# Performance work log

Measured on AMD Instinct MI355X. Metric: run time of the kernel, lower is better.

The kernel has to match this reference:

```python
import jax, jax.numpy as jnp
import numpy as np

N_NODES = 50000


def _sage_conv(x, src, dst, Wl, bl, Wr):
    # mean aggregation of source-node features into target nodes
    agg = jax.ops.segment_sum(x[src], dst, num_segments=N_NODES)      # [N, C]
    deg = jax.ops.segment_sum(jnp.ones_like(src, dtype=x.dtype), dst,
                              num_segments=N_NODES)                   # [N]
    mean = agg / jnp.maximum(deg, 1.0)[:, None]
    # PyG SAGEConv: lin_l(aggr) (with bias) + lin_r(x) (no bias)
    return mean @ Wl.T + bl + x @ Wr.T


def setup_inputs() -> dict:
    key = jax.random.key(0)
    ks = jax.random.split(key, 8)
    C = 128
    E = 600000
    scale = 1.0 / np.sqrt(C)
    x = jax.random.normal(ks[0], (N_NODES, C), dtype=jnp.float32)
    edge_index = jax.random.randint(ks[1], (2, E), 0, N_NODES, dtype=jnp.int64)
    Wl1 = jax.random.normal(ks[2], (C, C), dtype=jnp.float32) * scale
    bl1 = jnp.zeros((C,), dtype=jnp.float32)
    Wr1 = jax.random.normal(ks[3], (C, C), dtype=jnp.float32) * scale
    Wl2 = jax.random.normal(ks[4], (C, C), dtype=jnp.float32) * scale
    bl2 = jnp.zeros((C,), dtype=jnp.float32)
    Wr2 = jax.random.normal(ks[5], (C, C), dtype=jnp.float32) * scale
    return {"x": x, "edge_index": edge_index, "Wl1": Wl1, "bl1": bl1,
            "Wr1": Wr1, "Wl2": Wl2, "bl2": bl2, "Wr2": Wr2}


def reference(x, edge_index, Wl1, bl1, Wr1, Wl2, bl2, Wr2):
    src, dst = edge_index[0], edge_index[1]
    h = _sage_conv(x, src, dst, Wl1, bl1, Wr1)
    h = jax.nn.relu(h)
    out = _sage_conv(h, src, dst, Wl2, bl2, Wr2)
    return out
```

## Files before the change

kernel.cpp:

```cpp
#include <hip/hip_runtime.h>
#include <hip/hip_bf16.h>

#define N_NODES 50000
#define C 128
#define NPAD 50176
#define NTILES (NPAD / 16)
#define GEMM_BLOCKS (NTILES / 8)
#define SCAN1_BLOCKS (NPAD / 256)
#define XPREP_BLOCKS 3125
#define WPREP_BLOCKS 256

typedef short bf16x8 __attribute__((ext_vector_type(8)));
typedef float f32x4 __attribute__((ext_vector_type(4)));

__device__ __forceinline__ unsigned short f2bf(float f) {
    unsigned int u = __float_as_uint(f);
    unsigned int r = u + 0x7fffu + ((u >> 16) & 1u);
    return (unsigned short)(r >> 16);
}

__device__ __forceinline__ float bf2f(unsigned short b) {
    return __uint_as_float(((unsigned int)b) << 16);
}

__global__ __launch_bounds__(256) void build_kernel(
    const int* __restrict__ dst, int* __restrict__ deg, int E, int edgeBlocks,
    const float* __restrict__ x, unsigned short* __restrict__ Xb,
    const float* __restrict__ Wl1, const float* __restrict__ Wr1,
    const float* __restrict__ Wl2, const float* __restrict__ Wr2,
    unsigned short* __restrict__ Wc1, unsigned short* __restrict__ Wc2) {
    int b = blockIdx.x;
    if (b < edgeBlocks) {
        int e = b * 256 + threadIdx.x;
        if (e < E) {
            int d = dst[e];
            if ((unsigned)d < (unsigned)N_NODES) atomicAdd(deg + d, 1);
        }
    } else if (b < edgeBlocks + XPREP_BLOCKS) {
        int t = (b - edgeBlocks) * 256 + threadIdx.x;
        if (t >= N_NODES * C / 8) return;
        const float4 a = *(const float4*)(x + (size_t)t * 8);
        const float4 c = *(const float4*)(x + (size_t)t * 8 + 4);
        unsigned short o[8] = {f2bf(a.x), f2bf(a.y), f2bf(a.z), f2bf(a.w),
                               f2bf(c.x), f2bf(c.y), f2bf(c.z), f2bf(c.w)};
        *(uint4*)(Xb + (size_t)t * 8) = *(const uint4*)o;
    } else {
        int idx = (b - edgeBlocks - XPREP_BLOCKS) * 256 + threadIdx.x;
        int layer = idx >> 15;
        int r = idx & 32767;
        int j = r >> 8, k = r & 255;
        const float* Wl = layer ? Wl2 : Wl1;
        const float* Wr = layer ? Wr2 : Wr1;
        unsigned short* Wc = layer ? Wc2 : Wc1;
        float f = (k < 128) ? Wl[j * 128 + k] : Wr[j * 128 + (k - 128)];
        Wc[r] = f2bf(f);
    }
}

__global__ __launch_bounds__(256) void scan1_kernel(const int* __restrict__ deg,
                                                    int* __restrict__ scanbuf,
                                                    int* __restrict__ blocksum) {
    int i = blockIdx.x * 256 + threadIdx.x;
    int v = (i < N_NODES) ? deg[i] : 0;
    int lane = threadIdx.x & 63;
    int wv = threadIdx.x >> 6;
    int s = v;
#pragma unroll
    for (int off = 1; off < 64; off <<= 1) {
        int t = __shfl_up(s, off, 64);
        if (lane >= off) s += t;
    }
    __shared__ int wsum[4];
    if (lane == 63) wsum[wv] = s;
    __syncthreads();
    int woff = 0;
#pragma unroll
    for (int k = 0; k < 4; ++k) woff += (k < wv) ? wsum[k] : 0;
    scanbuf[i] = s + woff - v;
    if (threadIdx.x == 255) blocksum[blockIdx.x] = s + woff;
}

__global__ __launch_bounds__(256) void scan2_kernel(const int* __restrict__ blocksum,
                                                    int* __restrict__ blockoff) {
    int t = threadIdx.x;
    int v = (t < SCAN1_BLOCKS) ? blocksum[t] : 0;
    int lane = t & 63, wv = t >> 6;
    int s = v;
#pragma unroll
    for (int off = 1; off < 64; off <<= 1) {
        int tmp = __shfl_up(s, off, 64);
        if (lane >= off) s += tmp;
    }
    __shared__ int wsum[4];
    if (lane == 63) wsum[wv] = s;
    __syncthreads();
    int woff = 0;
#pragma unroll
    for (int k = 0; k < 4; ++k) woff += (k < wv) ? wsum[k] : 0;
    if (t < SCAN1_BLOCKS) blockoff[t] = s + woff - v;
}


__global__ void fill_kernel(const int* __restrict__ src, const int* __restrict__ dst,
                            const int* __restrict__ scanbuf, const int* __restrict__ blockoff,
                            int* __restrict__ cursor, int* __restrict__ csr_src, int E) {
    int e = blockIdx.x * 256 + threadIdx.x;
    if (e < E) {
        int d = dst[e];
        int s = src[e];
        if ((unsigned)d < (unsigned)N_NODES && (unsigned)s < (unsigned)N_NODES) {
            int rp = scanbuf[d] + blockoff[d >> 8];
            int pos = rp + atomicAdd(cursor + d, 1);
            csr_src[pos] = s;
        }
    }
}

__global__ __launch_bounds__(256) void gather_kernel(
    const unsigned short* __restrict__ feat,
    const int* __restrict__ scanbuf, const int* __restrict__ blockoff,
    const int* __restrict__ csr_src, unsigned short* __restrict__ Fm) {
    int w = (blockIdx.x * 256 + threadIdx.x) >> 6;
    int lane = threadIdx.x & 63;
    if (w >= N_NODES) return;
    const int beg = scanbuf[w] + blockoff[w >> 8];
    const int end = scanbuf[w + 1] + blockoff[(w + 1) >> 8];
    const int deg = end - beg;
    float ax = 0.f, ay = 0.f;
    const unsigned short* fp = feat + lane * 2;
    for (int base = beg; base < end; base += 64) {
        const int cnt = min(64, end - base);
        int myidx = 0;
        if (lane < cnt) myidx = csr_src[base + lane];
        int j = 0;
        for (; j + 3 < cnt; j += 4) {
            int s0 = __shfl(myidx, j);
            int s1 = __shfl(myidx, j + 1);
            int s2 = __shfl(myidx, j + 2);
            int s3 = __shfl(myidx, j + 3);
            unsigned int u0 = *(const unsigned int*)(fp + (size_t)s0 * C);
            unsigned int u1 = *(const unsigned int*)(fp + (size_t)s1 * C);
            unsigned int u2 = *(const unsigned int*)(fp + (size_t)s2 * C);
            unsigned int u3 = *(const unsigned int*)(fp + (size_t)s3 * C);
            ax += bf2f((unsigned short)u0) + bf2f((unsigned short)u1) +
                  bf2f((unsigned short)u2) + bf2f((unsigned short)u3);
            ay += bf2f((unsigned short)(u0 >> 16)) + bf2f((unsigned short)(u1 >> 16)) +
                  bf2f((unsigned short)(u2 >> 16)) + bf2f((unsigned short)(u3 >> 16));
        }
        for (; j < cnt; ++j) {
            int s0 = __shfl(myidx, j);
            unsigned int u0 = *(const unsigned int*)(fp + (size_t)s0 * C);
            ax += bf2f((unsigned short)u0);
            ay += bf2f((unsigned short)(u0 >> 16));
        }
    }
    const float inv = 1.0f / fmaxf((float)deg, 1.0f);
    unsigned int mpack = (unsigned)f2bf(ax * inv) | ((unsigned)f2bf(ay * inv) << 16);
    *(unsigned int*)(Fm + (size_t)w * C + lane * 2) = mpack;
}

__global__ __launch_bounds__(256) void sage_gemm(
    const unsigned short* __restrict__ Fm,
    const unsigned short* __restrict__ Self,
    const unsigned short* __restrict__ Wc,
    const float* __restrict__ bias,
    void* __restrict__ outv, int relu, int obf16) {
    __shared__ unsigned short wl[128 * 264];
    for (int cidx = threadIdx.x; cidx < 4096; cidx += 256) {
        int row = cidx >> 5, chunk = cidx & 31;
        const uint4 v = *(const uint4*)(Wc + row * 256 + chunk * 8);
        *(uint4*)(&wl[row * 264 + chunk * 8]) = v;
    }
    __syncthreads();

    const int wave = threadIdx.x >> 6;
    const int lane = threadIdx.x & 63;
    const int m = lane & 15;
    const int q = lane >> 4;
    const int tile0 = blockIdx.x * 8 + wave * 2;

    const size_t rowoff = (size_t)(tile0 * 16 + m) * C + q * 8;
    const unsigned short* am = Fm + rowoff;
    const unsigned short* as = Self + rowoff;

    f32x4 acc[2][8];
#pragma unroll
    for (int t = 0; t < 2; ++t)
#pragma unroll
        for (int j = 0; j < 8; ++j) acc[t][j] = (f32x4){0.f, 0.f, 0.f, 0.f};

#pragma unroll
    for (int kt = 0; kt < 8; ++kt) {
        const unsigned short* A = (kt < 4) ? am : as;
        const int ko = (kt & 3) * 32;
        bf16x8 af0 = *(const bf16x8*)(A + ko);
        bf16x8 af1 = *(const bf16x8*)(A + 16 * C + ko);
#pragma unroll
        for (int jt = 0; jt < 8; ++jt) {
            bf16x8 bfrag = *(const bf16x8*)(&wl[(jt * 16 + m) * 264 + kt * 32 + q * 8]);
            acc[0][jt] = __builtin_amdgcn_mfma_f32_16x16x32_bf16(af0, bfrag, acc[0][jt], 0, 0, 0);
            acc[1][jt] = __builtin_amdgcn_mfma_f32_16x16x32_bf16(af1, bfrag, acc[1][jt], 0, 0, 0);
        }
    }

#pragma unroll
    for (int t = 0; t < 2; ++t) {
        int rbase = (tile0 + t) * 16 + q * 4;
#pragma unroll
        for (int r = 0; r < 4; ++r) {
            int row = rbase + r;
            if (row < N_NODES) {
#pragma unroll
                for (int jt = 0; jt < 8; ++jt) {
                    int col = jt * 16 + m;
                    float v = acc[t][jt][r] + bias[col];
                    if (relu) v = fmaxf(v, 0.0f);
                    if (obf16)
                        ((unsigned short*)outv)[(size_t)row * C + col] = f2bf(v);
                    else
                        ((float*)outv)[(size_t)row * C + col] = v;
                }
            }
        }
    }
}

extern "C" void kernel_launch(void* const* d_in, const int* in_sizes, int n_in,
                              void* d_out, int out_size, void* d_ws, size_t ws_size,
                              hipStream_t stream) {
    const float* x = (const float*)d_in[0];
    const int* edge = (const int*)d_in[1];
    const float* Wl1 = (const float*)d_in[2];
    const float* bl1 = (const float*)d_in[3];
    const float* Wr1 = (const float*)d_in[4];
    const float* Wl2 = (const float*)d_in[5];
    const float* bl2 = (const float*)d_in[6];
    const float* Wr2 = (const float*)d_in[7];
    float* out = (float*)d_out;

    const int E = in_sizes[1] / 2;
    const int* src = edge;
    const int* dst = edge + E;

    char* ws = (char*)d_ws;
    size_t off = 0;
    int* deg = (int*)(ws + off);              off += (size_t)N_NODES * 4;
    int* cursor = (int*)(ws + off);           off += (size_t)N_NODES * 4;
    off = (off + 511) & ~511ull;
    int* scanbuf = (int*)(ws + off);          off += ((size_t)NPAD * 4 + 511) & ~511ull;
    int* blocksum = (int*)(ws + off);         off += 512 * 4;
    int* blockoff = (int*)(ws + off);         off += 512 * 4;
    int* csr_src = (int*)(ws + off);          off += ((size_t)E * 4 + 511) & ~511ull;
    unsigned short* Xb = (unsigned short*)(ws + off); off += (size_t)NPAD * C * 2;
    unsigned short* Fm = (unsigned short*)(ws + off); off += (size_t)NPAD * C * 2;
    unsigned short* h  = (unsigned short*)(ws + off); off += (size_t)NPAD * C * 2;
    unsigned short* Wc1 = (unsigned short*)(ws + off); off += 128 * 256 * 2;
    unsigned short* Wc2 = (unsigned short*)(ws + off); off += 128 * 256 * 2;
    (void)ws_size;

    const int edgeBlocks = (E + 255) / 256;
    const int gatherBlocks = (NPAD * 64) / 256;

    hipMemsetAsync(deg, 0, (size_t)N_NODES * 8, stream);
    build_kernel<<<edgeBlocks + XPREP_BLOCKS + WPREP_BLOCKS, 256, 0, stream>>>(
        dst, deg, E, edgeBlocks, x, Xb, Wl1, Wr1, Wl2, Wr2, Wc1, Wc2);
    scan1_kernel<<<SCAN1_BLOCKS, 256, 0, stream>>>(deg, scanbuf, blocksum);
    scan2_kernel<<<1, 256, 0, stream>>>(blocksum, blockoff);
    fill_kernel<<<edgeBlocks, 256, 0, stream>>>(src, dst, scanbuf, blockoff, cursor, csr_src, E);

    gather_kernel<<<gatherBlocks, 256, 0, stream>>>(Xb, scanbuf, blockoff, csr_src, Fm);
    sage_gemm<<<GEMM_BLOCKS, 256, 0, stream>>>(Fm, Xb, Wc1, bl1, h, 1, 1);

    gather_kernel<<<gatherBlocks, 256, 0, stream>>>(h, scanbuf, blockoff, csr_src, Fm);
    sage_gemm<<<GEMM_BLOCKS, 256, 0, stream>>>(Fm, h, Wc2, bl2, out, 0, 0);
}
```

Measured before the change: 244.3 us.

## Fuse neighbor-mean gather into SAGE GEMM via shared-memory mean tile

Merges the gather and GEMM kernels into one per-layer kernel. Each wave aggregates the mean features for its 32 rows into LDS, two nodes at a time over a combined edge range with 8-way unrolled loads, then runs the MFMA GEMM reading the mean from LDS and the weights straight from global memory instead of staging them in LDS. This removes the Fm round trip through global memory and two launches per forward. The cost is far fewer waves doing the gather (GEMM_BLOCKS×4 waves instead of one wave per node), so less latency hiding for the random gathers and more serial work per wave, plus weight fragments fetched from global/L2 on every iteration.

```diff
diff --git a/kernel.cpp b/kernel.cpp
--- a/kernel.cpp
+++ b/kernel.cpp
@@ -116,72 +116,73 @@
     }
 }
 
-__global__ __launch_bounds__(256) void gather_kernel(
+__global__ __launch_bounds__(256) void fused_layer(
     const unsigned short* __restrict__ feat,
     const int* __restrict__ scanbuf, const int* __restrict__ blockoff,
-    const int* __restrict__ csr_src, unsigned short* __restrict__ Fm) {
-    int w = (blockIdx.x * 256 + threadIdx.x) >> 6;
-    int lane = threadIdx.x & 63;
-    if (w >= N_NODES) return;
-    const int beg = scanbuf[w] + blockoff[w >> 8];
-    const int end = scanbuf[w + 1] + blockoff[(w + 1) >> 8];
-    const int deg = end - beg;
-    float ax = 0.f, ay = 0.f;
-    const unsigned short* fp = feat + lane * 2;
-    for (int base = beg; base < end; base += 64) {
-        const int cnt = min(64, end - base);
-        int myidx = 0;
-        if (lane < cnt) myidx = csr_src[base + lane];
-        int j = 0;
-        for (; j + 3 < cnt; j += 4) {
-            int s0 = __shfl(myidx, j);
-            int s1 = __shfl(myidx, j + 1);
-            int s2 = __shfl(myidx, j + 2);
-            int s3 = __shfl(myidx, j + 3);
-            unsigned int u0 = *(const unsigned int*)(fp + (size_t)s0 * C);
-            unsigned int u1 = *(const unsigned int*)(fp + (size_t)s1 * C);
-            unsigned int u2 = *(const unsigned int*)(fp + (size_t)s2 * C);
-            unsigned int u3 = *(const unsigned int*)(fp + (size_t)s3 * C);
-            ax += bf2f((unsigned short)u0) + bf2f((unsigned short)u1) +
-                  bf2f((unsigned short)u2) + bf2f((unsigned short)u3);
-            ay += bf2f((unsigned short)(u0 >> 16)) + bf2f((unsigned short)(u1 >> 16)) +
-                  bf2f((unsigned short)(u2 >> 16)) + bf2f((unsigned short)(u3 >> 16));
-        }
-        for (; j < cnt; ++j) {
-            int s0 = __shfl(myidx, j);
-            unsigned int u0 = *(const unsigned int*)(fp + (size_t)s0 * C);
-            ax += bf2f((unsigned short)u0);
-            ay += bf2f((unsigned short)(u0 >> 16));
-        }
-    }
-    const float inv = 1.0f / fmaxf((float)deg, 1.0f);
-    unsigned int mpack = (unsigned)f2bf(ax * inv) | ((unsigned)f2bf(ay * inv) << 16);
-    *(unsigned int*)(Fm + (size_t)w * C + lane * 2) = mpack;
-}
-
-__global__ __launch_bounds__(256) void sage_gemm(
-    const unsigned short* __restrict__ Fm,
-    const unsigned short* __restrict__ Self,
+    const int* __restrict__ csr_src,
     const unsigned short* __restrict__ Wc,
     const float* __restrict__ bias,
     void* __restrict__ outv, int relu, int obf16) {
-    __shared__ unsigned short wl[128 * 264];
-    for (int cidx = threadIdx.x; cidx < 4096; cidx += 256) {
-        int row = cidx >> 5, chunk = cidx & 31;
-        const uint4 v = *(const uint4*)(Wc + row * 256 + chunk * 8);
-        *(uint4*)(&wl[row * 264 + chunk * 8]) = v;
-    }
-    __syncthreads();
-
+    __shared__ unsigned short smean[128 * 136];
     const int wave = threadIdx.x >> 6;
     const int lane = threadIdx.x & 63;
+    const int tile0 = blockIdx.x * 8 + wave * 2;
+    const int row0 = tile0 * 16;
+    const int lrow0 = wave * 32;
+
+    const unsigned short* fp = feat + lane * 2;
+    for (int r = 0; r < 32; r += 2) {
+        const int n0 = row0 + r;
+        if (n0 >= N_NODES) {
+            *(unsigned int*)(&smean[(lrow0 + r) * 136 + lane * 2]) = 0u;
+            *(unsigned int*)(&smean[(lrow0 + r + 1) * 136 + lane * 2]) = 0u;
+            continue;
+        }
+        const int beg0 = scanbuf[n0] + blockoff[n0 >> 8];
+        const int mid  = scanbuf[n0 + 1] + blockoff[(n0 + 1) >> 8];
+        const int end1 = scanbuf[n0 + 2] + blockoff[(n0 + 2) >> 8];
+        float ax0 = 0.f, ay0 = 0.f, ax1 = 0.f, ay1 = 0.f;
+        for (int base = beg0; base < end1; base += 64) {
+            const int cnt = min(64, end1 - base);
+            int myidx = (lane < cnt) ? csr_src[base + lane] : 0;
+            int j = 0;
+            for (; j + 7 < cnt; j += 8) {
+                unsigned int u[8];
+#pragma unroll
+                for (int l = 0; l < 8; ++l) {
+                    int s = __shfl(myidx, j + l);
+                    u[l] = *(const unsigned int*)(fp + (size_t)s * C);
+                }
+#pragma unroll
+                for (int l = 0; l < 8; ++l) {
+                    float vx = bf2f((unsigned short)u[l]);
+                    float vy = bf2f((unsigned short)(u[l] >> 16));
+                    if (base + j + l < mid) { ax0 += vx; ay0 += vy; }
+                    else                    { ax1 += vx; ay1 += vy; }
+                }
+            }
+            for (; j < cnt; ++j) {
+                int s = __shfl(myidx, j);
+                unsigned int uu = *(const unsigned int*)(fp + (size_t)s * C);
+                float vx = bf2f((unsigned short)uu);
+                float vy = bf2f((unsigned short)(uu >> 16));
+                if (base + j < mid) { ax0 += vx; ay0 += vy; }
+                else                { ax1 += vx; ay1 += vy; }
+            }
+        }
+        const float inv0 = 1.0f / fmaxf((float)(mid - beg0), 1.0f);
+        const float inv1 = 1.0f / fmaxf((float)(end1 - mid), 1.0f);
+        unsigned int p0 = (unsigned)f2bf(ax0 * inv0) | ((unsigned)f2bf(ay0 * inv0) << 16);
+        unsigned int p1 = (unsigned)f2bf(ax1 * inv1) | ((unsigned)f2bf(ay1 * inv1) << 16);
+        *(unsigned int*)(&smean[(lrow0 + r) * 136 + lane * 2]) = p0;
+        *(unsigned int*)(&smean[(lrow0 + r + 1) * 136 + lane * 2]) = p1;
+    }
+    __syncthreads();
+
     const int m = lane & 15;
     const int q = lane >> 4;
-    const int tile0 = blockIdx.x * 8 + wave * 2;
-
-    const size_t rowoff = (size_t)(tile0 * 16 + m) * C + q * 8;
-    const unsigned short* am = Fm + rowoff;
-    const unsigned short* as = Self + rowoff;
+    const unsigned short* as = feat + (size_t)(row0 + m) * C + q * 8;
+    const unsigned short* lm = &smean[(lrow0 + m) * 136 + q * 8];
 
     f32x4 acc[2][8];
 #pragma unroll
@@ -191,13 +192,18 @@
 
 #pragma unroll
     for (int kt = 0; kt < 8; ++kt) {
-        const unsigned short* A = (kt < 4) ? am : as;
-        const int ko = (kt & 3) * 32;
-        bf16x8 af0 = *(const bf16x8*)(A + ko);
-        bf16x8 af1 = *(const bf16x8*)(A + 16 * C + ko);
+        bf16x8 af0, af1;
+        if (kt < 4) {
+            af0 = *(const bf16x8*)(lm + kt * 32);
+            af1 = *(const bf16x8*)(lm + 16 * 136 + kt * 32);
+        } else {
+            const int ko = (kt - 4) * 32;
+            af0 = *(const bf16x8*)(as + ko);
+            af1 = *(const bf16x8*)(as + 16 * C + ko);
+        }
 #pragma unroll
         for (int jt = 0; jt < 8; ++jt) {
-            bf16x8 bfrag = *(const bf16x8*)(&wl[(jt * 16 + m) * 264 + kt * 32 + q * 8]);
+            bf16x8 bfrag = *(const bf16x8*)(Wc + (jt * 16 + m) * 256 + kt * 32 + q * 8);
             acc[0][jt] = __builtin_amdgcn_mfma_f32_16x16x32_bf16(af0, bfrag, acc[0][jt], 0, 0, 0);
             acc[1][jt] = __builtin_amdgcn_mfma_f32_16x16x32_bf16(af1, bfrag, acc[1][jt], 0, 0, 0);
         }
@@ -252,14 +258,12 @@
     int* blockoff = (int*)(ws + off);         off += 512 * 4;
     int* csr_src = (int*)(ws + off);          off += ((size_t)E * 4 + 511) & ~511ull;
     unsigned short* Xb = (unsigned short*)(ws + off); off += (size_t)NPAD * C * 2;
-    unsigned short* Fm = (unsigned short*)(ws + off); off += (size_t)NPAD * C * 2;
     unsigned short* h  = (unsigned short*)(ws + off); off += (size_t)NPAD * C * 2;
     unsigned short* Wc1 = (unsigned short*)(ws + off); off += 128 * 256 * 2;
     unsigned short* Wc2 = (unsigned short*)(ws + off); off += 128 * 256 * 2;
     (void)ws_size;
 
     const int edgeBlocks = (E + 255) / 256;
-    const int gatherBlocks = (NPAD * 64) / 256;
 
     hipMemsetAsync(deg, 0, (size_t)N_NODES * 8, stream);
     build_kernel<<<edgeBlocks + XPREP_BLOCKS + WPREP_BLOCKS, 256, 0, stream>>>(
@@ -268,9 +272,8 @@
     scan2_kernel<<<1, 256, 0, stream>>>(blocksum, blockoff);
     fill_kernel<<<edgeBlocks, 256, 0, stream>>>(src, dst, scanbuf, blockoff, cursor, csr_src, E);
 
-    gather_kernel<<<gatherBlocks, 256, 0, stream>>>(Xb, scanbuf, blockoff, csr_src, Fm);
-    sage_gemm<<<GEMM_BLOCKS, 256, 0, stream>>>(Fm, Xb, Wc1, bl1, h, 1, 1);
-
-    gather_kernel<<<gatherBlocks, 256, 0, stream>>>(h, scanbuf, blockoff, csr_src, Fm);
-    sage_gemm<<<GEMM_BLOCKS, 256, 0, stream>>>(Fm, h, Wc2, bl2, out, 0, 0);
-}
+    fused_layer<<<GEMM_BLOCKS, 256, 0, stream>>>(Xb, scanbuf, blockoff, csr_src,
+                                                 Wc1, bl1, h, 1, 1);
+    fused_layer<<<GEMM_BLOCKS, 256, 0, stream>>>(h, scanbuf, blockoff, csr_src,
+                                                 Wc2, bl2, out, 0, 0);
+}
```

Result: slower. 322.8 us (+32.2%).

## Fuse whole GNN pipeline into one cooperative persistent kernel with grid syncs

Applied to the files above, without the earlier changes.

Replaces the eight separate launches plus memset with a single cooperative kernel of 512 blocks that steps through each stage in grid-stride loops separated by grid.sync(). The aim is to remove per-launch overhead and the idle gaps between the many small stages. It also unrolls the gather loop to 8 loads in flight and reads GEMM weight fragments straight from global memory instead of staging them in LDS. Risks are the cost of grid-wide barriers, lower parallelism in the gather phases from the fixed grid, and non-LDS weight reads. If the cooperative launch fails, the old multi-kernel path still runs.

```diff
diff --git a/kernel.cpp b/kernel.cpp
--- a/kernel.cpp
+++ b/kernel.cpp
@@ -1,12 +1,20 @@
 #include <hip/hip_runtime.h>
 #include <hip/hip_bf16.h>
+#include <hip/hip_cooperative_groups.h>
+
+namespace cg = cooperative_groups;
 
 #define N_NODES 50000
 #define C 128
 #define NPAD 50176
 #define NTILES (NPAD / 16)
 #define GEMM_BLOCKS (NTILES / 8)
-#define SCAN1_BLOCKS (NPAD / 256)
+#define SCAN_CHUNKS (NPAD / 256)
+#define GRID 512
+#define GWAVES (GRID * 4)
+#define XCHUNKS (N_NODES * C / 8)
+#define WITEMS (2 * 128 * 256)
+#define SCAN1_BLOCKS SCAN_CHUNKS
 #define XPREP_BLOCKS 3125
 #define WPREP_BLOCKS 256
 
@@ -22,6 +30,217 @@
 __device__ __forceinline__ float bf2f(unsigned short b) {
     return __uint_as_float(((unsigned int)b) << 16);
 }
+
+
+__device__ __forceinline__ void gather_one_node(
+    int w, int lane, const unsigned short* __restrict__ feat,
+    const int* __restrict__ scanbuf, const int* __restrict__ blockoff,
+    const int* __restrict__ csr_src, unsigned short* __restrict__ Fm) {
+    const int beg = scanbuf[w] + blockoff[w >> 8];
+    const int end = scanbuf[w + 1] + blockoff[(w + 1) >> 8];
+    float ax = 0.f, ay = 0.f;
+    const unsigned short* fp = feat + lane * 2;
+    for (int base = beg; base < end; base += 64) {
+        const int cnt = min(64, end - base);
+        int myidx = (lane < cnt) ? csr_src[base + lane] : 0;
+        int j = 0;
+        for (; j + 7 < cnt; j += 8) {
+            unsigned int u[8];
+#pragma unroll
+            for (int l = 0; l < 8; ++l) {
+                int s = __shfl(myidx, j + l);
+                u[l] = *(const unsigned int*)(fp + (size_t)s * C);
+            }
+#pragma unroll
+            for (int l = 0; l < 8; ++l) {
+                ax += bf2f((unsigned short)u[l]);
+                ay += bf2f((unsigned short)(u[l] >> 16));
+            }
+        }
+        for (; j < cnt; ++j) {
+            int s = __shfl(myidx, j);
+            unsigned int uu = *(const unsigned int*)(fp + (size_t)s * C);
+            ax += bf2f((unsigned short)uu);
+            ay += bf2f((unsigned short)(uu >> 16));
+        }
+    }
+    const float inv = 1.0f / fmaxf((float)(end - beg), 1.0f);
+    unsigned int mpack = (unsigned)f2bf(ax * inv) | ((unsigned)f2bf(ay * inv) << 16);
+    *(unsigned int*)(Fm + (size_t)w * C + lane * 2) = mpack;
+}
+
+__device__ __forceinline__ void gemm_tile(
+    int tile8, int wave, int lane,
+    const unsigned short* __restrict__ Fm, const unsigned short* __restrict__ Self,
+    const unsigned short* __restrict__ Wc, const float* __restrict__ bias,
+    void* __restrict__ outv, int relu, int obf16) {
+    const int m = lane & 15;
+    const int q = lane >> 4;
+    const int tile0 = tile8 * 8 + wave * 2;
+    const size_t rowoff = (size_t)(tile0 * 16 + m) * C + q * 8;
+    const unsigned short* am = Fm + rowoff;
+    const unsigned short* as = Self + rowoff;
+
+    f32x4 acc[2][8];
+#pragma unroll
+    for (int t = 0; t < 2; ++t)
+#pragma unroll
+        for (int j = 0; j < 8; ++j) acc[t][j] = (f32x4){0.f, 0.f, 0.f, 0.f};
+
+#pragma unroll
+    for (int kt = 0; kt < 8; ++kt) {
+        const unsigned short* A = (kt < 4) ? am : as;
+        const int ko = (kt & 3) * 32;
+        bf16x8 af0 = *(const bf16x8*)(A + ko);
+        bf16x8 af1 = *(const bf16x8*)(A + 16 * C + ko);
+#pragma unroll
+        for (int jt = 0; jt < 8; ++jt) {
+            bf16x8 bfrag = *(const bf16x8*)(Wc + (jt * 16 + m) * 256 + kt * 32 + q * 8);
+            acc[0][jt] = __builtin_amdgcn_mfma_f32_16x16x32_bf16(af0, bfrag, acc[0][jt], 0, 0, 0);
+            acc[1][jt] = __builtin_amdgcn_mfma_f32_16x16x32_bf16(af1, bfrag, acc[1][jt], 0, 0, 0);
+        }
+    }
+
+#pragma unroll
+    for (int t = 0; t < 2; ++t) {
+        int rbase = (tile0 + t) * 16 + q * 4;
+#pragma unroll
+        for (int r = 0; r < 4; ++r) {
+            int row = rbase + r;
+            if (row < N_NODES) {
+#pragma unroll
+                for (int jt = 0; jt < 8; ++jt) {
+                    int col = jt * 16 + m;
+                    float v = acc[t][jt][r] + bias[col];
+                    if (relu) v = fmaxf(v, 0.0f);
+                    if (obf16)
+                        ((unsigned short*)outv)[(size_t)row * C + col] = f2bf(v);
+                    else
+                        ((float*)outv)[(size_t)row * C + col] = v;
+                }
+            }
+        }
+    }
+}
+
+
+struct GnnParams {
+    const int* src; const int* dst; int E;
+    const float* x;
+    const float* Wl1; const float* bl1; const float* Wr1;
+    const float* Wl2; const float* bl2; const float* Wr2;
+    float* out;
+    int* deg; int* cursor; int* scanbuf; int* blocksum; int* blockoff; int* csr_src;
+    unsigned short* Xb; unsigned short* Fm; unsigned short* h;
+    unsigned short* Wc1; unsigned short* Wc2;
+};
+
+__global__ __launch_bounds__(256, 2) void mega_kernel(GnnParams p) {
+    __shared__ int wsum[4];
+    cg::grid_group grid = cg::this_grid();
+    const int gtid = blockIdx.x * 256 + threadIdx.x;
+    const int gstride = GRID * 256;
+    const int tid = threadIdx.x;
+    const int wave = tid >> 6;
+    const int lane = tid & 63;
+    const int gw = gtid >> 6;
+
+    for (int g = gtid; g < 2 * N_NODES; g += gstride) p.deg[g] = 0;
+    grid.sync();
+
+    {
+        const int tot1 = p.E;
+        const int tot2 = tot1 + XCHUNKS;
+        const int tot3 = tot2 + WITEMS;
+        for (int g = gtid; g < tot3; g += gstride) {
+            if (g < tot1) {
+                int d = p.dst[g];
+                if ((unsigned)d < (unsigned)N_NODES) atomicAdd(p.deg + d, 1);
+            } else if (g < tot2) {
+                int t = g - tot1;
+                const float4 a = *(const float4*)(p.x + (size_t)t * 8);
+                const float4 c = *(const float4*)(p.x + (size_t)t * 8 + 4);
+                unsigned short o[8] = {f2bf(a.x), f2bf(a.y), f2bf(a.z), f2bf(a.w),
+                                       f2bf(c.x), f2bf(c.y), f2bf(c.z), f2bf(c.w)};
+                *(uint4*)(p.Xb + (size_t)t * 8) = *(const uint4*)o;
+            } else {
+                int idx = g - tot2;
+                int layer = idx >> 15;
+                int r = idx & 32767;
+                int j = r >> 8, k = r & 255;
+                const float* Wl = layer ? p.Wl2 : p.Wl1;
+                const float* Wr = layer ? p.Wr2 : p.Wr1;
+                unsigned short* Wc = layer ? p.Wc2 : p.Wc1;
+                float f = (k < 128) ? Wl[j * 128 + k] : Wr[j * 128 + (k - 128)];
+                Wc[r] = f2bf(f);
+            }
+        }
+    }
+    grid.sync();
+
+    if (blockIdx.x < SCAN_CHUNKS) {
+        int i = blockIdx.x * 256 + tid;
+        int v = (i < N_NODES) ? p.deg[i] : 0;
+        int s = v;
+#pragma unroll
+        for (int off = 1; off < 64; off <<= 1) {
+            int t = __shfl_up(s, off, 64);
+            if (lane >= off) s += t;
+        }
+        if (lane == 63) wsum[wave] = s;
+        __syncthreads();
+        int woff = 0;
+#pragma unroll
+        for (int k = 0; k < 4; ++k) woff += (k < wave) ? wsum[k] : 0;
+        p.scanbuf[i] = s + woff - v;
+        if (tid == 255) p.blocksum[blockIdx.x] = s + woff;
+    }
+    grid.sync();
+
+    if (blockIdx.x == 0) {
+        int v = (tid < SCAN_CHUNKS) ? p.blocksum[tid] : 0;
+        int s = v;
+#pragma unroll
+        for (int off = 1; off < 64; off <<= 1) {
+            int tmp = __shfl_up(s, off, 64);
+            if (lane >= off) s += tmp;
+        }
+        if (lane == 63) wsum[wave] = s;
+        __syncthreads();
+        int woff = 0;
+#pragma unroll
+        for (int k = 0; k < 4; ++k) woff += (k < wave) ? wsum[k] : 0;
+        if (tid < SCAN_CHUNKS) p.blockoff[tid] = s + woff - v;
+    }
+    grid.sync();
+
+    for (int e = gtid; e < p.E; e += gstride) {
+        int d = p.dst[e];
+        int s = p.src[e];
+        if ((unsigned)d < (unsigned)N_NODES && (unsigned)s < (unsigned)N_NODES) {
+            int rp = p.scanbuf[d] + p.blockoff[d >> 8];
+            int pos = rp + atomicAdd(p.cursor + d, 1);
+            p.csr_src[pos] = s;
+        }
+    }
+    grid.sync();
+
+    for (int w = gw; w < N_NODES; w += GWAVES)
+        gather_one_node(w, lane, p.Xb, p.scanbuf, p.blockoff, p.csr_src, p.Fm);
+    grid.sync();
+
+    for (int t8 = blockIdx.x; t8 < GEMM_BLOCKS; t8 += GRID)
+        gemm_tile(t8, wave, lane, p.Fm, p.Xb, p.Wc1, p.bl1, p.h, 1, 1);
+    grid.sync();
+
+    for (int w = gw; w < N_NODES; w += GWAVES)
+        gather_one_node(w, lane, p.h, p.scanbuf, p.blockoff, p.csr_src, p.Fm);
+    grid.sync();
+
+    for (int t8 = blockIdx.x; t8 < GEMM_BLOCKS; t8 += GRID)
+        gemm_tile(t8, wave, lane, p.Fm, p.h, p.Wc2, p.bl2, p.out, 0, 0);
+}
+
 
 __global__ __launch_bounds__(256) void build_kernel(
     const int* __restrict__ dst, int* __restrict__ deg, int E, int edgeBlocks,
@@ -100,7 +319,6 @@
     if (t < SCAN1_BLOCKS) blockoff[t] = s + woff - v;
 }
 
-
 __global__ void fill_kernel(const int* __restrict__ src, const int* __restrict__ dst,
                             const int* __restrict__ scanbuf, const int* __restrict__ blockoff,
                             int* __restrict__ cursor, int* __restrict__ csr_src, int E) {
@@ -123,154 +341,72 @@
     int w = (blockIdx.x * 256 + threadIdx.x) >> 6;
     int lane = threadIdx.x & 63;
     if (w >= N_NODES) return;
-    const int beg = scanbuf[w] + blockoff[w >> 8];
-    const int end = scanbuf[w + 1] + blockoff[(w + 1) >> 8];
-    const int deg = end - beg;
-    float ax = 0.f, ay = 0.f;
-    const unsigned short* fp = feat + lane * 2;
-    for (int base = beg; base < end; base += 64) {
-        const int cnt = min(64, end - base);
-        int myidx = 0;
-        if (lane < cnt) myidx = csr_src[base + lane];
-        int j = 0;
-        for (; j + 3 < cnt; j += 4) {
-            int s0 = __shfl(myidx, j);
-            int s1 = __shfl(myidx, j + 1);
-            int s2 = __shfl(myidx, j + 2);
-            int s3 = __shfl(myidx, j + 3);
-            unsigned int u0 = *(const unsigned int*)(fp + (size_t)s0 * C);
-            unsigned int u1 = *(const unsigned int*)(fp + (size_t)s1 * C);
-            unsigned int u2 = *(const unsigned int*)(fp + (size_t)s2 * C);
-            unsigned int u3 = *(const unsigned int*)(fp + (size_t)s3 * C);
-            ax += bf2f((unsigned short)u0) + bf2f((unsigned short)u1) +
-                  bf2f((unsigned short)u2) + bf2f((unsigned short)u3);
-            ay += bf2f((unsigned short)(u0 >> 16)) + bf2f((unsigned short)(u1 >> 16)) +
-                  bf2f((unsigned short)(u2 >> 16)) + bf2f((unsigned short)(u3 >> 16));
-        }
-        for (; j < cnt; ++j) {
-            int s0 = __shfl(myidx, j);
-            unsigned int u0 = *(const unsigned int*)(fp + (size_t)s0 * C);
-            ax += bf2f((unsigned short)u0);
-            ay += bf2f((unsigned short)(u0 >> 16));
-        }
-    }
-    const float inv = 1.0f / fmaxf((float)deg, 1.0f);
-    unsigned int mpack = (unsigned)f2bf(ax * inv) | ((unsigned)f2bf(ay * inv) << 16);
-    *(unsigned int*)(Fm + (size_t)w * C + lane * 2) = mpack;
+    gather_one_node(w, lane, feat, scanbuf, blockoff, csr_src, Fm);
 }
 
 __global__ __launch_bounds__(256) void sage_gemm(
-    const unsigned short* __restrict__ Fm,
-    const unsigned short* __restrict__ Self,
-    const unsigned short* __restrict__ Wc,
-    const float* __restrict__ bias,
+    const unsigned short* __restrict__ Fm, const unsigned short* __restrict__ Self,
+    const unsigned short* __restrict__ Wc, const float* __restrict__ bias,
     void* __restrict__ outv, int relu, int obf16) {
-    __shared__ unsigned short wl[128 * 264];
-    for (int cidx = threadIdx.x; cidx < 4096; cidx += 256) {
-        int row = cidx >> 5, chunk = cidx & 31;
-        const uint4 v = *(const uint4*)(Wc + row * 256 + chunk * 8);
-        *(uint4*)(&wl[row * 264 + chunk * 8]) = v;
-    }
-    __syncthreads();
-
-    const int wave = threadIdx.x >> 6;
-    const int lane = threadIdx.x & 63;
-    const int m = lane & 15;
-    const int q = lane >> 4;
-    const int tile0 = blockIdx.x * 8 + wave * 2;
-
-    const size_t rowoff = (size_t)(tile0 * 16 + m) * C + q * 8;
-    const unsigned short* am = Fm + rowoff;
-    const unsigned short* as = Self + rowoff;
-
-    f32x4 acc[2][8];
-#pragma unroll
-    for (int t = 0; t < 2; ++t)
-#pragma unroll
-        for (int j = 0; j < 8; ++j) acc[t][j] = (f32x4){0.f, 0.f, 0.f, 0.f};
-
-#pragma unroll
-    for (int kt = 0; kt < 8; ++kt) {
-        const unsigned short* A = (kt < 4) ? am : as;
-        const int ko = (kt & 3) * 32;
-        bf16x8 af0 = *(const bf16x8*)(A + ko);
-        bf16x8 af1 = *(const bf16x8*)(A + 16 * C + ko);
-#pragma unroll
-        for (int jt = 0; jt < 8; ++jt) {
-            bf16x8 bfrag = *(const bf16x8*)(&wl[(jt * 16 + m) * 264 + kt * 32 + q * 8]);
-            acc[0][jt] = __builtin_amdgcn_mfma_f32_16x16x32_bf16(af0, bfrag, acc[0][jt], 0, 0, 0);
-            acc[1][jt] = __builtin_amdgcn_mfma_f32_16x16x32_bf16(af1, bfrag, acc[1][jt], 0, 0, 0);
-        }
-    }
-
-#pragma unroll
-    for (int t = 0; t < 2; ++t) {
-        int rbase = (tile0 + t) * 16 + q * 4;
-#pragma unroll
-        for (int r = 0; r < 4; ++r) {
-            int row = rbase + r;
-            if (row < N_NODES) {
-#pragma unroll
-                for (int jt = 0; jt < 8; ++jt) {
-                    int col = jt * 16 + m;
-                    float v = acc[t][jt][r] + bias[col];
-                    if (relu) v = fmaxf(v, 0.0f);
-                    if (obf16)
-                        ((unsigned short*)outv)[(size_t)row * C + col] = f2bf(v);
-                    else
-                        ((float*)outv)[(size_t)row * C + col] = v;
-                }
-            }
-        }
-    }
-}
+    gemm_tile(blockIdx.x, threadIdx.x >> 6, threadIdx.x & 63,
+              Fm, Self, Wc, bias, outv, relu, obf16);
+}
+
 
 extern "C" void kernel_launch(void* const* d_in, const int* in_sizes, int n_in,
                               void* d_out, int out_size, void* d_ws, size_t ws_size,
                               hipStream_t stream) {
-    const float* x = (const float*)d_in[0];
+    const int E = in_sizes[1] / 2;
     const int* edge = (const int*)d_in[1];
-    const float* Wl1 = (const float*)d_in[2];
-    const float* bl1 = (const float*)d_in[3];
-    const float* Wr1 = (const float*)d_in[4];
-    const float* Wl2 = (const float*)d_in[5];
-    const float* bl2 = (const float*)d_in[6];
-    const float* Wr2 = (const float*)d_in[7];
-    float* out = (float*)d_out;
-
-    const int E = in_sizes[1] / 2;
-    const int* src = edge;
-    const int* dst = edge + E;
+
+    GnnParams p;
+    p.src = edge;
+    p.dst = edge + E;
+    p.E = E;
+    p.x   = (const float*)d_in[0];
+    p.Wl1 = (const float*)d_in[2];
+    p.bl1 = (const float*)d_in[3];
+    p.Wr1 = (const float*)d_in[4];
+    p.Wl2 = (const float*)d_in[5];
+    p.bl2 = (const float*)d_in[6];
+    p.Wr2 = (const float*)d_in[7];
+    p.out = (float*)d_out;
 
     char* ws = (char*)d_ws;
     size_t off = 0;
-    int* deg = (int*)(ws + off);              off += (size_t)N_NODES * 4;
-    int* cursor = (int*)(ws + off);           off += (size_t)N_NODES * 4;
+    p.deg = (int*)(ws + off);              off += (size_t)N_NODES * 4;
+    p.cursor = (int*)(ws + off);           off += (size_t)N_NODES * 4;
     off = (off + 511) & ~511ull;
-    int* scanbuf = (int*)(ws + off);          off += ((size_t)NPAD * 4 + 511) & ~511ull;
-    int* blocksum = (int*)(ws + off);         off += 512 * 4;
-    int* blockoff = (int*)(ws + off);         off += 512 * 4;
-    int* csr_src = (int*)(ws + off);          off += ((size_t)E * 4 + 511) & ~511ull;
-    unsigned short* Xb = (unsigned short*)(ws + off); off += (size_t)NPAD * C * 2;
-    unsigned short* Fm = (unsigned short*)(ws + off); off += (size_t)NPAD * C * 2;
-    unsigned short* h  = (unsigned short*)(ws + off); off += (size_t)NPAD * C * 2;
-    unsigned short* Wc1 = (unsigned short*)(ws + off); off += 128 * 256 * 2;
-    unsigned short* Wc2 = (unsigned short*)(ws + off); off += 128 * 256 * 2;
+    p.scanbuf = (int*)(ws + off);          off += ((size_t)NPAD * 4 + 511) & ~511ull;
+    p.blocksum = (int*)(ws + off);         off += 512 * 4;
+    p.blockoff = (int*)(ws + off);         off += 512 * 4;
+    p.csr_src = (int*)(ws + off);          off += ((size_t)E * 4 + 511) & ~511ull;
+    p.Xb = (unsigned short*)(ws + off);    off += (size_t)NPAD * C * 2;
+    p.Fm = (unsigned short*)(ws + off);    off += (size_t)NPAD * C * 2;
+    p.h  = (unsigned short*)(ws + off);    off += (size_t)NPAD * C * 2;
+    p.Wc1 = (unsigned short*)(ws + off);   off += 128 * 256 * 2;
+    p.Wc2 = (unsigned short*)(ws + off);   off += 128 * 256 * 2;
     (void)ws_size;
+
+    void* args[] = {(void*)&p};
+    hipError_t err = hipLaunchCooperativeKernel((void*)mega_kernel, dim3(GRID),
+                                                dim3(256), args, 0, stream);
+    if (err == hipSuccess) return;
 
     const int edgeBlocks = (E + 255) / 256;
     const int gatherBlocks = (NPAD * 64) / 256;
 
-    hipMemsetAsync(deg, 0, (size_t)N_NODES * 8, stream);
+    hipMemsetAsync(p.deg, 0, (size_t)N_NODES * 8, stream);
     build_kernel<<<edgeBlocks + XPREP_BLOCKS + WPREP_BLOCKS, 256, 0, stream>>>(
-        dst, deg, E, edgeBlocks, x, Xb, Wl1, Wr1, Wl2, Wr2, Wc1, Wc2);
-    scan1_kernel<<<SCAN1_BLOCKS, 256, 0, stream>>>(deg, scanbuf, blocksum);
-    scan2_kernel<<<1, 256, 0, stream>>>(blocksum, blockoff);
-    fill_kernel<<<edgeBlocks, 256, 0, stream>>>(src, dst, scanbuf, blockoff, cursor, csr_src, E);
-
-    gather_kernel<<<gatherBlocks, 256, 0, stream>>>(Xb, scanbuf, blockoff, csr_src, Fm);
-    sage_gemm<<<GEMM_BLOCKS, 256, 0, stream>>>(Fm, Xb, Wc1, bl1, h, 1, 1);
-
-    gather_kernel<<<gatherBlocks, 256, 0, stream>>>(h, scanbuf, blockoff, csr_src, Fm);
-    sage_gemm<<<GEMM_BLOCKS, 256, 0, stream>>>(Fm, h, Wc2, bl2, out, 0, 0);
-}
+        p.dst, p.deg, E, edgeBlocks, p.x, p.Xb, p.Wl1, p.Wr1, p.Wl2, p.Wr2, p.Wc1, p.Wc2);
+    scan1_kernel<<<SCAN1_BLOCKS, 256, 0, stream>>>(p.deg, p.scanbuf, p.blocksum);
+    scan2_kernel<<<1, 256, 0, stream>>>(p.blocksum, p.blockoff);
+    fill_kernel<<<edgeBlocks, 256, 0, stream>>>(p.src, p.dst, p.scanbuf, p.blockoff,
+                                                p.cursor, p.csr_src, E);
+    gather_kernel<<<gatherBlocks, 256, 0, stream>>>(p.Xb, p.scanbuf, p.blockoff,
+                                                    p.csr_src, p.Fm);
+    sage_gemm<<<GEMM_BLOCKS, 256, 0, stream>>>(p.Fm, p.Xb, p.Wc1, p.bl1, p.h, 1, 1);
+    gather_kernel<<<gatherBlocks, 256, 0, stream>>>(p.h, p.scanbuf, p.blockoff,
+                                                    p.csr_src, p.Fm);
+    sage_gemm<<<GEMM_BLOCKS, 256, 0, stream>>>(p.Fm, p.h, p.Wc2, p.bl2, p.out, 0, 0);
+}
```

Result: slower. 819.2 us (+235.3%).
